# Optimization experiments

Measured on AMD Instinct MI355X. Metric: run time of the kernel, lower is better.

The kernel has to match this reference:

```python
import jax, jax.numpy as jnp
import numpy as np

B, T, F, L, E, H, A, V = 64, 32, 512, 196, 512, 512, 512, 10000


def setup_inputs() -> dict:
    key = jax.random.key(0)
    ks = jax.random.split(key, 24)
    s = 0.02
    features = jax.random.normal(ks[0], (B, F, L), dtype=jnp.float32)
    captions = jax.random.randint(ks[1], (B, T), 0, V)
    lengths = jnp.sort(jax.random.randint(ks[2], (B,), 2, T + 1))[::-1]
    lengths = lengths.at[0].set(T)  # ensure max(decode_lengths) == T-1 (static)
    return {
        "features": features,
        "captions": captions,
        "lengths": lengths,
        "W_emb": jax.random.normal(ks[3], (V, E)) * s,
        "W_enc": jax.random.normal(ks[4], (A, F)) * s,
        "b_enc": jnp.zeros((A,)),
        "W_dec": jax.random.normal(ks[5], (A, H)) * s,
        "b_dec": jnp.zeros((A,)),
        "W_full": jax.random.normal(ks[6], (1, A)) * s,
        "b_full": jnp.zeros((1,)),
        "W_fbeta": jax.random.normal(ks[7], (F, H)) * s,
        "b_fbeta": jnp.zeros((F,)),
        "W_ih": jax.random.normal(ks[8], (4 * H, E + F)) * s,
        "W_hh": jax.random.normal(ks[9], (4 * H, H)) * s,
        "b_ih": jnp.zeros((4 * H,)),
        "b_hh": jnp.zeros((4 * H,)),
        "W_out": jax.random.normal(ks[10], (V, H)) * s,
        "b_out": jnp.zeros((V,)),
        "W_init_h": jax.random.normal(ks[11], (H, F)) * s,
        "b_init_h": jnp.zeros((H,)),
        "W_init_c": jax.random.normal(ks[12], (H, F)) * s,
        "b_init_c": jnp.zeros((H,)),
    }


def reference(features, captions, lengths, W_emb, W_enc, b_enc, W_dec, b_dec,
              W_full, b_full, W_fbeta, b_fbeta, W_ih, W_hh, b_ih, b_hh,
              W_out, b_out, W_init_h, b_init_h, W_init_c, b_init_c):
    Bv, Fv, Lv = features.shape
    Tmax = captions.shape[1] - 1  # max(decode_lengths), static (lengths[0]==T)
    feat_r = features.reshape(Bv, -1, Fv)          # [B, L, F] (torch .view semantics)
    en_att = feat_r @ W_enc.T + b_enc              # [B, L, A], step-invariant
    mean_f = features.mean(axis=2)                 # [B, F]
    h0 = mean_f @ W_init_h.T + b_init_h            # [B, H]
    c0 = mean_f @ W_init_c.T + b_init_c
    emb = W_emb[captions]                          # [B, T, E]
    dec_len = lengths - 1                          # [B]

    def step(carry, xs):
        h, c = carry
        emb_t, i = xs
        de = h @ W_dec.T + b_dec                                   # [B, A]
        full = (jnp.tanh(en_att + de[:, None, :]) @ W_full.T)[..., 0] + b_full[0]  # [B, L]
        alpha = jax.nn.softmax(full, axis=1)                       # [B, L]
        z = jnp.einsum('blf,bl->bf', feat_r, alpha)                # [B, F]
        z = z * jax.nn.sigmoid(h @ W_fbeta.T + b_fbeta)
        x = jnp.concatenate([emb_t, z], axis=1)                    # [B, E+F]
        gates = x @ W_ih.T + b_ih + h @ W_hh.T + b_hh              # [B, 4H]
        ig, fg, gg, og = jnp.split(gates, 4, axis=1)
        c_new = jax.nn.sigmoid(fg) * c + jax.nn.sigmoid(ig) * jnp.tanh(gg)
        h_new = jax.nn.sigmoid(og) * jnp.tanh(c_new)
        out = h_new @ W_out.T + b_out                              # [B, V] (dropout: eval)
        active = (dec_len > i)[:, None]                            # ragged mask
        h = jnp.where(active, h_new, h)
        c = jnp.where(active, c_new, c)
        pred = jnp.where(active, out, 0.0)
        alpha_m = jnp.where(active, alpha, 0.0)
        return (h, c), (pred, alpha_m)

    emb_steps = jnp.swapaxes(emb[:, :Tmax, :], 0, 1)               # [Tmax, B, E]
    (_, _), (preds, alphas) = jax.lax.scan(step, (h0, c0), (emb_steps, jnp.arange(Tmax)))
    predictions = jnp.swapaxes(preds, 0, 1)                        # [B, Tmax, V]
    alphas = jnp.swapaxes(alphas, 0, 1)                            # [B, Tmax, L]
    return predictions, alphas
```

## Files before the change

kernel.cpp:

```cpp
#include <hip/hip_runtime.h>


typedef unsigned short ushort_t;
typedef __attribute__((ext_vector_type(8))) short short8;
typedef __attribute__((ext_vector_type(4))) float f32x4;

__device__ __forceinline__ float bf2f(ushort_t u) {
    unsigned x = ((unsigned)u) << 16;
    float f;
    __builtin_memcpy(&f, &x, 4);
    return f;
}
__device__ __forceinline__ ushort_t f2bf(float f) {
    unsigned x;
    __builtin_memcpy(&x, &f, 4);
    unsigned r = (x + 0x7fffu + ((x >> 16) & 1u)) >> 16;
    return (ushort_t)r;
}
__device__ __forceinline__ float sigmoidf_(float x) { return 1.f / (1.f + __expf(-x)); }
__device__ __forceinline__ float tanh_fast(float x) {
    float e = __expf(2.f * x);
    return 1.f - 2.f / (e + 1.f);
}
__device__ __forceinline__ float wred_sum(float v) {
    #pragma unroll
    for (int m = 32; m; m >>= 1) v += __shfl_xor(v, m, 64);
    return v;
}
__device__ __forceinline__ float wred_max(float v) {
    #pragma unroll
    for (int m = 32; m; m >>= 1) v = fmaxf(v, __shfl_xor(v, m, 64));
    return v;
}

__device__ __forceinline__ float aload_f(const float* p) {
    return __hip_atomic_load((float*)p, __ATOMIC_RELAXED, __HIP_MEMORY_SCOPE_AGENT);
}
__device__ __forceinline__ void astore_f(float* p, float v) {
    __hip_atomic_store(p, v, __ATOMIC_RELAXED, __HIP_MEMORY_SCOPE_AGENT);
}
__device__ __forceinline__ unsigned aload_u(const unsigned* p) {
    return __hip_atomic_load((unsigned*)p, __ATOMIC_RELAXED, __HIP_MEMORY_SCOPE_AGENT);
}
__device__ __forceinline__ void astore_u(unsigned* p, unsigned v) {
    __hip_atomic_store(p, v, __ATOMIC_RELAXED, __HIP_MEMORY_SCOPE_AGENT);
}
__device__ __forceinline__ int aload_i(const int* p) {
    return __hip_atomic_load((int*)p, __ATOMIC_RELAXED, __HIP_MEMORY_SCOPE_AGENT);
}
__device__ __forceinline__ void astore_i(int* p, int v) {
    __hip_atomic_store(p, v, __ATOMIC_RELAXED, __HIP_MEMORY_SCOPE_AGENT);
}

#define KEXP2 2.8853901817779268f

__global__ void detect_kernel(const unsigned* __restrict__ feat_raw, int* __restrict__ flag,
                              int* __restrict__ flags) {
    int lane = threadIdx.x;
    #pragma unroll
    for (int i = 0; i < 8; ++i) flags[lane + i * 64] = 0;
    unsigned u = feat_raw[lane];
    unsigned e = (u >> 7) & 0xffu;
    bool bf_like = (e >= 105 && e <= 133);
    unsigned long long m = __ballot(bf_like);
    if (lane == 0) *flag = (__popcll(m) >= 40) ? 0 : 1;
}

#define NCVT 19
struct CvtArgs {
    const void* src[NCVT];
    void* dst[NCVT];
    int n[NCVT];
};

__global__ __launch_bounds__(256) void convert_kernel(CvtArgs a, const int* __restrict__ flag) {
    const int ai = blockIdx.y;
    const int n = a.n[ai];
    const int base = (blockIdx.x * 256 + threadIdx.x) * 8;
    if (base >= n) return;
    ushort_t* dst = (ushort_t*)a.dst[ai];
    if (*flag) {
        const float* s = (const float*)a.src[ai];
        #pragma unroll
        for (int i = 0; i < 8; ++i) {
            int idx = base + i;
            if (idx < n) dst[idx] = f2bf(s[idx]);
        }
    } else {
        const ushort_t* s = (const ushort_t*)a.src[ai];
        #pragma unroll
        for (int i = 0; i < 8; ++i) {
            int idx = base + i;
            if (idx < n) dst[idx] = s[idx];
        }
    }
}

__global__ __launch_bounds__(256) void embrows_kernel(const void* __restrict__ Wemb,
                                                      const int* __restrict__ captions,
                                                      const int* __restrict__ flag,
                                                      ushort_t* __restrict__ emb_c) {
    const int tb = blockIdx.x;
    const int t = tb >> 6, b = tb & 63;
    const int cap = captions[b * 32 + t];
    const int e0 = threadIdx.x;
    if (*flag) {
        const float* s = (const float*)Wemb + cap * 512;
        emb_c[tb * 512 + e0] = f2bf(s[e0]);
        emb_c[tb * 512 + e0 + 256] = f2bf(s[e0 + 256]);
    } else {
        const ushort_t* s = (const ushort_t*)Wemb + cap * 512;
        emb_c[tb * 512 + e0] = s[e0];
        emb_c[tb * 512 + e0 + 256] = s[e0 + 256];
    }
}

__global__ void prepw2_kernel(const ushort_t* __restrict__ wf, const ushort_t* __restrict__ bfc,
                              float* __restrict__ w2) {
    int tid = threadIdx.x;
    float w = bf2f(wf[tid]);
    w2[tid] = -2.f * w;
    float s = wred_sum(w);
    __shared__ float r8[8];
    if ((tid & 63) == 0) r8[tid >> 6] = s;
    __syncthreads();
    if (tid == 0) {
        float tot = r8[0] + r8[1] + r8[2] + r8[3] + r8[4] + r8[5] + r8[6] + r8[7];
        w2[512] = tot + bf2f(bfc[0]);
    }
}

template <class AROW, class BROW, class EPI>
__device__ __forceinline__ void gemm_tile(AROW arow, BROW brow, EPI epi) {
    __shared__ __align__(16) ushort_t As[64][40];
    __shared__ __align__(16) ushort_t Bs[64][40];
    const int tid = threadIdx.x;
    const int row = tid >> 2, ks = (tid & 3) << 3;
    const int wave = tid >> 6, lane = tid & 63;
    const int quad = lane >> 4, l15 = lane & 15;
    f32x4 acc[4];
    #pragma unroll
    for (int s = 0; s < 4; ++s) acc[s] = (f32x4){0.f, 0.f, 0.f, 0.f};
    const ushort_t* ap = arow(row);
    const ushort_t* bp = brow(row);
    for (int k0 = 0; k0 < 512; k0 += 32) {
        short8 av = {0, 0, 0, 0, 0, 0, 0, 0};
        short8 bv = {0, 0, 0, 0, 0, 0, 0, 0};
        if (ap) av = *(const short8*)(ap + k0 + ks);
        if (bp) bv = *(const short8*)(bp + k0 + ks);
        __syncthreads();
        *(short8*)&As[row][ks] = av;
        *(short8*)&Bs[row][ks] = bv;
        __syncthreads();
        short8 af = *(const short8*)&As[(wave << 4) + l15][quad << 3];
        #pragma unroll
        for (int s = 0; s < 4; ++s) {
            short8 bfr = *(const short8*)&Bs[(s << 4) + l15][quad << 3];
            acc[s] = __builtin_amdgcn_mfma_f32_16x16x32_bf16(af, bfr, acc[s], 0, 0, 0);
        }
    }
    epi((wave << 4) + (quad << 2), l15, acc);
}

__global__ __launch_bounds__(256) void mean_kernel(const ushort_t* __restrict__ features,
                                                   ushort_t* __restrict__ mean_bf) {
    const int b = blockIdx.x;
    const int wave = threadIdx.x >> 6, lane = threadIdx.x & 63;
    const ushort_t* fb = features + b * 512 * 196;
    for (int f = wave; f < 512; f += 4) {
        const ushort_t* r = fb + f * 196;
        float s = bf2f(r[lane]) + bf2f(r[lane + 64]) + bf2f(r[lane + 128]);
        if (lane < 4) s += bf2f(r[lane + 192]);
        s = wred_sum(s);
        if (lane == 0) mean_bf[b * 512 + f] = f2bf(s * (1.f / 196.f));
    }
}

__global__ __launch_bounds__(256) void init_kernel(
    const ushort_t* __restrict__ mean_bf, const ushort_t* __restrict__ Winh,
    const ushort_t* __restrict__ binh, const ushort_t* __restrict__ Winc,
    const ushort_t* __restrict__ binc, ushort_t* __restrict__ h_bf,
    float* __restrict__ cbuf) {
    const int n0 = blockIdx.x << 6;
    gemm_tile(
        [&](int r) { return mean_bf + r * 512; },
        [&](int r) {
            int n = n0 + r;
            return (n < 512) ? (Winh + n * 512) : (Winc + (n - 512) * 512);
        },
        [&](int mb, int l15, const f32x4* acc) {
            #pragma unroll
            for (int s = 0; s < 4; ++s) {
                int n = n0 + (s << 4) + l15;
                #pragma unroll
                for (int r = 0; r < 4; ++r) {
                    int b = mb + r;
                    if (n < 512)
                        h_bf[b * 512 + n] = f2bf(acc[s][r] + bf2f(binh[n]));
                    else
                        cbuf[b * 512 + (n - 512)] = acc[s][r] + bf2f(binc[n - 512]);
                }
            }
        });
}

__global__ __launch_bounds__(256) void enatt_kernel(const ushort_t* __restrict__ feat,
                                                    const ushort_t* __restrict__ Wenc,
                                                    const ushort_t* __restrict__ benc,
                                                    ushort_t* __restrict__ en_att) {
    const int m0 = blockIdx.y << 6, n0 = blockIdx.x << 6;
    gemm_tile(
        [&](int r) { return feat + (m0 + r) * 512; },
        [&](int r) { return Wenc + (n0 + r) * 512; },
        [&](int mb, int l15, const f32x4* acc) {
            #pragma unroll
            for (int s = 0; s < 4; ++s) {
                int n = n0 + (s << 4) + l15;
                float bias = bf2f(benc[n]);
                #pragma unroll
                for (int r = 0; r < 4; ++r) {
                    int m = m0 + mb + r;
                    en_att[m * 512 + n] = f2bf(acc[s][r] + bias);
                }
            }
        });
}

__global__ __launch_bounds__(256) void ec_kernel(const ushort_t* __restrict__ emb_c,
                                                 const ushort_t* __restrict__ Wih,
                                                 const ushort_t* __restrict__ bih,
                                                 const ushort_t* __restrict__ bhh,
                                                 float* __restrict__ ec) {
    const int t = blockIdx.y, n0 = blockIdx.x << 6;
    gemm_tile(
        [&](int r) { return emb_c + (t * 64 + r) * 512; },
        [&](int r) { return Wih + (n0 + r) * 1024; },
        [&](int mb, int l15, const f32x4* acc) {
            #pragma unroll
            for (int s = 0; s < 4; ++s) {
                int j = n0 + (s << 4) + l15;
                float bias = bf2f(bih[j]) + bf2f(bhh[j]);
                #pragma unroll
                for (int r = 0; r < 4; ++r) {
                    int b = mb + r;
                    ec[(t * 64 + b) * 2048 + j] = acc[s][r] + bias;
                }
            }
        });
}

struct LoopArgs {
    const ushort_t* W3c;
    const ushort_t* bdec;
    const ushort_t* bfb;
    const ushort_t* en_att;
    const ushort_t* feat;
    const ushort_t* Wih;
    const float* w2;
    const float* ec;
    const int* lengths;
    const int* flag;
    ushort_t* h_bf;
    ushort_t* z_bf;
    ushort_t* H_all;
    float* cbuf;
    float* deK;
    float* fgate;
    float* hh;
    void* out_base;
    int* flags;
};

__global__ __launch_bounds__(512, 2) void loop_kernel(LoopArgs A) {
    const int blk = blockIdx.x, tid = threadIdx.x;
    const int wave = tid >> 6, lane = tid & 63;
    const int quad = lane >> 4, l15 = lane & 15;
    const int g = blk >> 6, local = blk & 63;
    int* fbase = A.flags + g * 128;

    __shared__ __align__(16) ushort_t enS[49 * 512];
    __shared__ __align__(16) ushort_t ftS[196 * 128];
    __shared__ __align__(16) ushort_t AsL[16][520];
    __shared__ float smem[2048];
    __shared__ float fullS[200];
    __shared__ float red8[16];

    const int f32o = *A.flag;
    const int b0 = g << 4;
    const int Tg = A.lengths[b0] - 1;

    const bool roleA = local < 24;
    const int bB = b0 + (local >> 2);
    const int qB = local & 3;
    const int lenB = A.lengths[bB];
    const bool roleC = local < 32;
    const int dtC = local;

    unsigned* h_u32 = (unsigned*)A.h_bf;
    unsigned* z_u32 = (unsigned*)A.z_bf;

    float w2r[8];
    {
        f32x4 w0 = *(const f32x4*)(A.w2 + lane * 8);
        f32x4 w1 = *(const f32x4*)(A.w2 + lane * 8 + 4);
        w2r[0] = w0[0]; w2r[1] = w0[1]; w2r[2] = w0[2]; w2r[3] = w0[3];
        w2r[4] = w1[0]; w2r[5] = w1[1]; w2r[6] = w1[2]; w2r[7] = w1[3];
    }
    const float fullc = A.w2[512];

    {
        const short8* src = (const short8*)(A.en_att + ((size_t)bB * 196 + qB * 49) * 512);
        short8* dst = (short8*)enS;
        for (int i = tid; i < 49 * 64; i += 512) dst[i] = src[i];
        const ushort_t* fsrc = A.feat + (size_t)bB * 100352 + qB * 128;
        short8* fdst = (short8*)ftS;
        for (int i = tid; i < 196 * 16; i += 512) {
            int l = i >> 4, c = i & 15;
            fdst[i] = *(const short8*)(fsrc + l * 512 + c * 8);
        }
    }

    for (int t = 0; t < Tg; ++t) {
        if (roleA) {
            if (wave == 0 && t > 0) {
                const int* fp = fbase + (lane & 31);
                for (;;) {
                    if (__all(aload_i(fp) >= t)) break;
                    __builtin_amdgcn_s_sleep(1);
                }
                asm volatile("" ::: "memory");
            }
            __syncthreads();
            for (int i = tid; i < 4096; i += 512) {
                int r = i >> 8, c = i & 255;
                *(unsigned*)&AsL[r][c << 1] = aload_u(h_u32 + ((b0 + r) << 8) + c);
            }
            __syncthreads();
            const int nt = local * 8 + wave;
            const ushort_t* br = A.W3c + ((nt << 4) + l15) * 512 + (quad << 3);
            const ushort_t* arl = &AsL[l15][quad << 3];
            f32x4 acc = {0.f, 0.f, 0.f, 0.f};
            #pragma unroll
            for (int k0 = 0; k0 < 512; k0 += 32)
                acc = __builtin_amdgcn_mfma_f32_16x16x32_bf16(
                    *(const short8*)(arl + k0), *(const short8*)(br + k0), acc, 0, 0, 0);
            const int n = (nt << 4) + l15;
            #pragma unroll
            for (int r = 0; r < 4; ++r) {
                const int b = b0 + (quad << 2) + r;
                float v = acc[r];
                if (n < 512)
                    astore_f(A.deK + b * 512 + n, (v + bf2f(A.bdec[n])) * KEXP2);
                else if (n < 1024)
                    astore_f(A.fgate + b * 512 + (n - 512),
                             sigmoidf_(v + bf2f(A.bfb[n - 512])));
                else
                    astore_f(A.hh + b * 2048 + (n - 1024), v);
            }
            asm volatile("s_waitcnt vmcnt(0)" ::: "memory");
            __syncthreads();
            if (tid == 0) astore_i(fbase + 32 + local, t + 1);
        }

        {
            if (wave == 0) {
                const int* fp = fbase + 32 + (lane & 7);
                for (;;) {
                    if (__all(aload_i(fp) >= t + 1)) break;
                    __builtin_amdgcn_s_sleep(1);
                }
                asm volatile("" ::: "memory");
            }
            __syncthreads();
            const bool act = (lenB - 1) > t;
            const size_t aoff = 19840000ull + ((size_t)bB * 31 + t) * 196;
            if (act) {
                float dkr[8];
                const float* dk = A.deK + bB * 512 + lane * 8;
                #pragma unroll
                for (int j = 0; j < 8; ++j) dkr[j] = aload_f(dk + j);
                const ushort_t* enb = A.en_att + (size_t)bB * 100352;
                const int lp0 = qB * 49;
                for (int l = wave; l < 196; l += 8) {
                    const ushort_t* er = (l >= lp0 && l < lp0 + 49)
                                             ? (enS + (l - lp0) * 512)
                                             : (enb + l * 512);
                    short8 ev = *(const short8*)(er + lane * 8);
                    float acc = 0.f;
                    #pragma unroll
                    for (int j = 0; j < 8; ++j) {
                        float e2 = __builtin_amdgcn_exp2f(
                            fmaf(bf2f((ushort_t)ev[j]), KEXP2, dkr[j]));
                        acc = fmaf(w2r[j], __builtin_amdgcn_rcpf(e2 + 1.f), acc);
                    }
                    acc = wred_sum(acc);
                    if (lane == 0) fullS[l] = acc + fullc;
                }
                __syncthreads();
                float v = (tid < 196) ? fullS[tid] : -1e30f;
                float wm = wred_max(v);
                if (lane == 0) red8[wave] = wm;
                __syncthreads();
                float mx = fmaxf(fmaxf(fmaxf(red8[0], red8[1]), fmaxf(red8[2], red8[3])),
                                 fmaxf(fmaxf(red8[4], red8[5]), fmaxf(red8[6], red8[7])));
                float e = (tid < 196) ? __expf(v - mx) : 0.f;
                float sw = wred_sum(e);
                if (lane == 0) red8[8 + wave] = sw;
                __syncthreads();
                float tot = red8[8] + red8[9] + red8[10] + red8[11] +
                            red8[12] + red8[13] + red8[14] + red8[15];
                float inv = 1.f / tot;
                float a = e * inv;
                if (tid < 196) {
                    fullS[tid] = a;
                    if (qB == 0) {
                        if (f32o) ((float*)A.out_base)[aoff + tid] = a;
                        else ((ushort_t*)A.out_base)[aoff + tid] = f2bf(a);
                    }
                }
                __syncthreads();
                const int fl = tid & 127, gq = tid >> 7;
                float zacc = 0.f;
                #pragma unroll 4
                for (int l = gq; l < 196; l += 4)
                    zacc = fmaf(fullS[l], bf2f(ftS[l * 128 + fl]), zacc);
                smem[256 + (gq << 7) + fl] = zacc;
                __syncthreads();
                if (tid < 64) {
                    const int f0l = tid << 1;
                    float z0 = smem[256 + f0l] + smem[384 + f0l] +
                               smem[512 + f0l] + smem[640 + f0l];
                    float z1 = smem[257 + f0l] + smem[385 + f0l] +
                               smem[513 + f0l] + smem[641 + f0l];
                    const int f0 = (qB << 7) + f0l;
                    z0 *= aload_f(A.fgate + bB * 512 + f0);
                    z1 *= aload_f(A.fgate + bB * 512 + f0 + 1);
                    unsigned zp = (unsigned)f2bf(z0) | ((unsigned)f2bf(z1) << 16);
                    astore_u(z_u32 + bB * 256 + (f0 >> 1), zp);
                }
            } else {
                if (qB == 0 && tid < 196) {
                    if (f32o) ((float*)A.out_base)[aoff + tid] = 0.f;
                    else ((ushort_t*)A.out_base)[aoff + tid] = 0;
                }
            }
            asm volatile("s_waitcnt vmcnt(0)" ::: "memory");
            __syncthreads();
            if (tid == 0) astore_i(fbase + 64 + local, t + 1);
        }

        if (roleC) {
            if (wave == 0) {
                const int* zp = fbase + 64 + lane;
                for (;;) {
                    int v1 = aload_i(zp);
                    int v2 = (lane < 4)
                                 ? aload_i(fbase + 32 + 8 + lane * 4 + (dtC >> 3))
                                 : 0x7fffffff;
                    if (__all(v1 >= t + 1 && v2 >= t + 1)) break;
                    __builtin_amdgcn_s_sleep(1);
                }
                asm volatile("" ::: "memory");
            }
            __syncthreads();
            float pe[8], ph[8];
            #pragma unroll
            for (int k = 0; k < 8; ++k) { pe[k] = 0.f; ph[k] = 0.f; }
            if (tid < 128) {
                const int bl = tid >> 3, p = tid & 7;
                const int bE = b0 + bl;
                const int dimE = (dtC << 4) + (p << 1);
                const int eb = (t * 64 + bE) * 2048, hb = bE * 2048;
                pe[0] = A.ec[eb + dimE];         pe[1] = A.ec[eb + dimE + 1];
                pe[2] = A.ec[eb + 512 + dimE];   pe[3] = A.ec[eb + 512 + dimE + 1];
                pe[4] = A.ec[eb + 1024 + dimE];  pe[5] = A.ec[eb + 1024 + dimE + 1];
                pe[6] = A.ec[eb + 1536 + dimE];  pe[7] = A.ec[eb + 1536 + dimE + 1];
                ph[0] = aload_f(A.hh + hb + dimE);
                ph[1] = aload_f(A.hh + hb + dimE + 1);
                ph[2] = aload_f(A.hh + hb + 512 + dimE);
                ph[3] = aload_f(A.hh + hb + 512 + dimE + 1);
                ph[4] = aload_f(A.hh + hb + 1024 + dimE);
                ph[5] = aload_f(A.hh + hb + 1024 + dimE + 1);
                ph[6] = aload_f(A.hh + hb + 1536 + dimE);
                ph[7] = aload_f(A.hh + hb + 1536 + dimE + 1);
            }
            for (int i = tid; i < 4096; i += 512) {
                int r = i >> 8, c = i & 255;
                *(unsigned*)&AsL[r][c << 1] = aload_u(z_u32 + ((b0 + r) << 8) + c);
            }
            __syncthreads();
            const int gw = wave & 3, kh = wave >> 2;
            const int j = (gw << 9) + (dtC << 4) + l15;
            const ushort_t* br = A.Wih + j * 1024 + 512 + (kh << 8) + (quad << 3);
            const ushort_t* arl = &AsL[l15][(kh << 8) + (quad << 3)];
            f32x4 acc = {0.f, 0.f, 0.f, 0.f};
            #pragma unroll
            for (int k0 = 0; k0 < 256; k0 += 32)
                acc = __builtin_amdgcn_mfma_f32_16x16x32_bf16(
                    *(const short8*)(arl + k0), *(const short8*)(br + k0), acc, 0, 0, 0);
            #pragma unroll
            for (int r = 0; r < 4; ++r)
                smem[(wave << 8) + (((quad << 2) + r) << 4) + l15] = acc[r];
            __syncthreads();
            if (tid < 128) {
                const int bl = tid >> 3, p = tid & 7;
                const int b = b0 + bl;
                const int i0 = (bl << 4) + (p << 1);
                const int dim = (dtC << 4) + (p << 1);
                float ig0 = smem[i0] + smem[1024 + i0] + pe[0] + ph[0];
                float ig1 = smem[i0 + 1] + smem[1025 + i0] + pe[1] + ph[1];
                float fg0 = smem[256 + i0] + smem[1280 + i0] + pe[2] + ph[2];
                float fg1 = smem[257 + i0] + smem[1281 + i0] + pe[3] + ph[3];
                float gg0 = smem[512 + i0] + smem[1536 + i0] + pe[4] + ph[4];
                float gg1 = smem[513 + i0] + smem[1537 + i0] + pe[5] + ph[5];
                float og0 = smem[768 + i0] + smem[1792 + i0] + pe[6] + ph[6];
                float og1 = smem[769 + i0] + smem[1793 + i0] + pe[7] + ph[7];
                float co0 = A.cbuf[b * 512 + dim];
                float co1 = A.cbuf[b * 512 + dim + 1];
                float cn0 = sigmoidf_(fg0) * co0 + sigmoidf_(ig0) * tanh_fast(gg0);
                float hn0 = sigmoidf_(og0) * tanh_fast(cn0);
                float cn1 = sigmoidf_(fg1) * co1 + sigmoidf_(ig1) * tanh_fast(gg1);
                float hn1 = sigmoidf_(og1) * tanh_fast(cn1);
                unsigned hp = (unsigned)f2bf(hn0) | ((unsigned)f2bf(hn1) << 16);
                *(unsigned*)&A.H_all[(t * 64 + b) * 512 + dim] = hp;
                if (A.lengths[b] - 1 > t) {
                    A.cbuf[b * 512 + dim] = cn0;
                    A.cbuf[b * 512 + dim + 1] = cn1;
                    astore_u(h_u32 + b * 256 + (dim >> 1), hp);
                }
            }
            asm volatile("s_waitcnt vmcnt(0)" ::: "memory");
            __syncthreads();
            if (tid == 0) astore_i(fbase + dtC, t + 1);
        }
    }

    if (qB == 0) {
        for (int t = Tg; t < 31; ++t) {
            if (tid < 196) {
                const size_t aoff = 19840000ull + ((size_t)bB * 31 + t) * 196;
                if (f32o) ((float*)A.out_base)[aoff + tid] = 0.f;
                else ((ushort_t*)A.out_base)[aoff + tid] = 0;
            }
        }
    }
}

__global__ __launch_bounds__(256) void preds_kernel(
    const ushort_t* __restrict__ H_all, const ushort_t* __restrict__ Wout,
    const ushort_t* __restrict__ bout, const int* __restrict__ lengths,
    const int* __restrict__ flag, void* __restrict__ out_base) {
    const int t = blockIdx.x, n0 = blockIdx.y << 6;
    const int f32o = *flag;
    gemm_tile(
        [&](int r) { return H_all + (t * 64 + r) * 512; },
        [&](int r) -> const ushort_t* {
            int n = n0 + r;
            return (n < 10000) ? (Wout + n * 512) : (const ushort_t*)nullptr;
        },
        [&](int mb, int l15, const f32x4* acc) {
            #pragma unroll
            for (int s = 0; s < 4; ++s) {
                int n = n0 + (s << 4) + l15;
                if (n >= 10000) continue;
                float bias = bf2f(bout[n]);
                #pragma unroll
                for (int r = 0; r < 4; ++r) {
                    int b = mb + r;
                    bool act = lengths[b] > t + 1;
                    float val = act ? (acc[s][r] + bias) : 0.f;
                    size_t off = (size_t)b * 310000 + t * 10000 + n;
                    if (f32o) ((float*)out_base)[off] = val;
                    else ((ushort_t*)out_base)[off] = act ? f2bf(val) : (ushort_t)0;
                }
            }
        });
}

extern "C" void kernel_launch(void* const* d_in, const int* in_sizes, int n_in,
                              void* d_out, int out_size, void* d_ws, size_t ws_size,
                              hipStream_t stream) {
    const void* features = d_in[0];
    const int* captions = (const int*)d_in[1];
    const int* lengths = (const int*)d_in[2];
    const void* W_emb = d_in[3];

    char* ws = (char*)d_ws;
    size_t o = 0;
    auto alloc = [&](size_t bytes) {
        size_t r = o;
        o += (bytes + 255) & ~(size_t)255;
        return r;
    };
    ushort_t* feat_c  = (ushort_t*)(ws + alloc(6422528ull * 2));
    ushort_t* Wenc_c  = (ushort_t*)(ws + alloc(262144ull * 2));
    ushort_t* benc_c  = (ushort_t*)(ws + alloc(512 * 2));
    ushort_t* W3c     = (ushort_t*)(ws + alloc(3072ull * 512 * 2));
    ushort_t* bdec_c  = (ushort_t*)(ws + alloc(512 * 2));
    ushort_t* wfull_c = (ushort_t*)(ws + alloc(512 * 2));
    ushort_t* bfull_c = (ushort_t*)(ws + alloc(2));
    ushort_t* bfb_c   = (ushort_t*)(ws + alloc(512 * 2));
    ushort_t* Wih_c   = (ushort_t*)(ws + alloc(2097152ull * 2));
    ushort_t* bih_c   = (ushort_t*)(ws + alloc(2048 * 2));
    ushort_t* bhh_c   = (ushort_t*)(ws + alloc(2048 * 2));
    ushort_t* Wout_c  = (ushort_t*)(ws + alloc(5120000ull * 2));
    ushort_t* bout_c  = (ushort_t*)(ws + alloc(10000 * 2));
    ushort_t* Winh_c  = (ushort_t*)(ws + alloc(262144ull * 2));
    ushort_t* binh_c  = (ushort_t*)(ws + alloc(512 * 2));
    ushort_t* Winc_c  = (ushort_t*)(ws + alloc(262144ull * 2));
    ushort_t* binc_c  = (ushort_t*)(ws + alloc(512 * 2));
    ushort_t* emb_c   = (ushort_t*)(ws + alloc(1984ull * 512 * 2));
    ushort_t* en_att  = (ushort_t*)(ws + alloc(12544ull * 512 * 2));
    float*    ec      = (float*)(ws + alloc(1984ull * 2048 * 4));
    ushort_t* H_all   = (ushort_t*)(ws + alloc(1984ull * 512 * 2));
    ushort_t* h_bf    = (ushort_t*)(ws + alloc(64 * 512 * 2));
    float*    cbuf    = (float*)(ws + alloc(64 * 512 * 4));
    float*    deK     = (float*)(ws + alloc(64 * 512 * 4));
    float*    fgate   = (float*)(ws + alloc(64 * 512 * 4));
    float*    hh      = (float*)(ws + alloc(64ull * 2048 * 4));
    ushort_t* z_bf    = (ushort_t*)(ws + alloc(64 * 512 * 2));
    ushort_t* mean_bf = (ushort_t*)(ws + alloc(64 * 512 * 2));
    float*    w2buf   = (float*)(ws + alloc(513 * 4));
    int*      flag    = (int*)(ws + alloc(256));
    int*      flags   = (int*)(ws + alloc(512 * 4));

    detect_kernel<<<1, 64, 0, stream>>>((const unsigned*)features, flag, flags);

    CvtArgs ca;
    const void* srcs[NCVT] = {features, d_in[4], d_in[5], d_in[6], d_in[7], d_in[8],
                              d_in[9], d_in[10], d_in[11], d_in[12], d_in[13], d_in[14],
                              d_in[15], d_in[16], d_in[17], d_in[18], d_in[19], d_in[20],
                              d_in[21]};
    void* dsts[NCVT] = {feat_c, Wenc_c, benc_c, W3c , bdec_c, wfull_c, bfull_c,
                        W3c + 262144 , bfb_c, Wih_c, W3c + 524288 ,
                        bih_c, bhh_c, Wout_c, bout_c, Winh_c, binh_c, Winc_c, binc_c};
    int ns[NCVT] = {6422528, 262144, 512, 262144, 512, 512, 1, 262144, 512,
                    2097152, 1048576, 2048, 2048, 5120000, 10000, 262144, 512,
                    262144, 512};
    for (int i = 0; i < NCVT; ++i) {
        ca.src[i] = srcs[i];
        ca.dst[i] = dsts[i];
        ca.n[i] = ns[i];
    }
    convert_kernel<<<dim3(3136, NCVT), 256, 0, stream>>>(ca, flag);
    embrows_kernel<<<1984, 256, 0, stream>>>(W_emb, captions, flag, emb_c);
    prepw2_kernel<<<1, 512, 0, stream>>>(wfull_c, bfull_c, w2buf);

    mean_kernel<<<64, 256, 0, stream>>>(feat_c, mean_bf);
    init_kernel<<<16, 256, 0, stream>>>(mean_bf, Winh_c, binh_c, Winc_c, binc_c,
                                        h_bf, cbuf);
    enatt_kernel<<<dim3(8, 196), 256, 0, stream>>>(feat_c, Wenc_c, benc_c, en_att);
    ec_kernel<<<dim3(32, 31), 256, 0, stream>>>(emb_c, Wih_c, bih_c, bhh_c, ec);

    LoopArgs la;
    la.W3c = W3c; la.bdec = bdec_c; la.bfb = bfb_c;
    la.en_att = en_att; la.feat = feat_c; la.Wih = Wih_c;
    la.w2 = w2buf; la.ec = ec; la.lengths = lengths; la.flag = flag;
    la.h_bf = h_bf; la.z_bf = z_bf; la.H_all = H_all;
    la.cbuf = cbuf; la.deK = deK; la.fgate = fgate; la.hh = hh;
    la.out_base = d_out; la.flags = flags;
    loop_kernel<<<256, 512, 0, stream>>>(la);

    preds_kernel<<<dim3(31, 157), 256, 0, stream>>>(H_all, Wout_c, bout_c, lengths,
                                                    flag, d_out);
}
```

Baseline: 1.454 ms.

## Split attention score computation across four blocks per batch row with flag sync

Before, each of the four blocks per batch row computed all 196 attention scores, reading three quarters of en_att from global memory. Now each block computes only the 49 scores whose en_att rows sit in its shared memory and writes them to a global fullv buffer. The four blocks then exchange readiness through new per-block flags and spin-wait before each reads the full 196-score vector for the softmax. This removes redundant exp/rcp work and global loads, at the cost of an extra inter-block barrier every timestep.

Result: faster. 1.177 ms (-19.1%).

```diff
diff --git a/kernel.cpp b/kernel.cpp
--- a/kernel.cpp
+++ b/kernel.cpp
@@ -58,7 +58,7 @@
                               int* __restrict__ flags) {
     int lane = threadIdx.x;
     #pragma unroll
-    for (int i = 0; i < 8; ++i) flags[lane + i * 64] = 0;
+    for (int i = 0; i < 16; ++i) flags[lane + i * 64] = 0;
     unsigned u = feat_raw[lane];
     unsigned e = (u >> 7) & 0xffu;
     bool bf_like = (e >= 105 && e <= 133);
@@ -267,6 +267,7 @@
     float* deK;
     float* fgate;
     float* hh;
+    float* fullv;
     void* out_base;
     int* flags;
 };
@@ -276,7 +277,7 @@
     const int wave = tid >> 6, lane = tid & 63;
     const int quad = lane >> 4, l15 = lane & 15;
     const int g = blk >> 6, local = blk & 63;
-    int* fbase = A.flags + g * 128;
+    int* fbase = A.flags + g * 256;
 
     __shared__ __align__(16) ushort_t enS[49 * 512];
     __shared__ __align__(16) ushort_t ftS[196 * 128];
@@ -379,13 +380,8 @@
                 const float* dk = A.deK + bB * 512 + lane * 8;
                 #pragma unroll
                 for (int j = 0; j < 8; ++j) dkr[j] = aload_f(dk + j);
-                const ushort_t* enb = A.en_att + (size_t)bB * 100352;
-                const int lp0 = qB * 49;
-                for (int l = wave; l < 196; l += 8) {
-                    const ushort_t* er = (l >= lp0 && l < lp0 + 49)
-                                             ? (enS + (l - lp0) * 512)
-                                             : (enb + l * 512);
-                    short8 ev = *(const short8*)(er + lane * 8);
+                for (int i = wave; i < 49; i += 8) {
+                    short8 ev = *(const short8*)(enS + i * 512 + lane * 8);
                     float acc = 0.f;
                     #pragma unroll
                     for (int j = 0; j < 8; ++j) {
@@ -394,10 +390,24 @@
                         acc = fmaf(w2r[j], __builtin_amdgcn_rcpf(e2 + 1.f), acc);
                     }
                     acc = wred_sum(acc);
-                    if (lane == 0) fullS[l] = acc + fullc;
-                }
-                __syncthreads();
-                float v = (tid < 196) ? fullS[tid] : -1e30f;
+                    if (lane == 0)
+                        astore_f(A.fullv + bB * 196 + qB * 49 + i, acc + fullc);
+                }
+            }
+            asm volatile("s_waitcnt vmcnt(0)" ::: "memory");
+            __syncthreads();
+            if (tid == 0) astore_i(fbase + 128 + local, t + 1);
+            if (wave == 0) {
+                const int* fp = fbase + 128 + (local & ~3) + (lane & 3);
+                for (;;) {
+                    if (__all(aload_i(fp) >= t + 1)) break;
+                    __builtin_amdgcn_s_sleep(1);
+                }
+                asm volatile("" ::: "memory");
+            }
+            __syncthreads();
+            if (act) {
+                float v = (tid < 196) ? aload_f(A.fullv + bB * 196 + tid) : -1e30f;
                 float wm = wred_max(v);
                 if (lane == 0) red8[wave] = wm;
                 __syncthreads();
@@ -620,9 +630,10 @@
     float*    hh      = (float*)(ws + alloc(64ull * 2048 * 4));
     ushort_t* z_bf    = (ushort_t*)(ws + alloc(64 * 512 * 2));
     ushort_t* mean_bf = (ushort_t*)(ws + alloc(64 * 512 * 2));
+    float*    fullv   = (float*)(ws + alloc(64 * 196 * 4));
     float*    w2buf   = (float*)(ws + alloc(513 * 4));
     int*      flag    = (int*)(ws + alloc(256));
-    int*      flags   = (int*)(ws + alloc(512 * 4));
+    int*      flags   = (int*)(ws + alloc(1024 * 4));
 
     detect_kernel<<<1, 64, 0, stream>>>((const unsigned*)features, flag, flags);
 
@@ -658,7 +669,7 @@
     la.w2 = w2buf; la.ec = ec; la.lengths = lengths; la.flag = flag;
     la.h_bf = h_bf; la.z_bf = z_bf; la.H_all = H_all;
     la.cbuf = cbuf; la.deK = deK; la.fgate = fgate; la.hh = hh;
-    la.out_base = d_out; la.flags = flags;
+    la.fullv = fullv; la.out_base = d_out; la.flags = flags;
     loop_kernel<<<256, 512, 0, stream>>>(la);
 
     preds_kernel<<<dim3(31, 157), 256, 0, stream>>>(H_all, Wout_c, bout_c, lengths,
```
